# Kernel optimization log

Hardware: AMD Instinct MI355X
Metric: run time of the kernel (lower is better)

## Reference

```python
import jax, jax.numpy as jnp
import numpy as np

DIM, HID = 32, 128
B, H, W = 2, 64, 64

def conv2d(x, w, b=None, pad=0, groups=1):
    out = jax.lax.conv_general_dilated(x, w, (1, 1), [(pad, pad), (pad, pad)],
        dimension_numbers=('NCHW', 'OIHW', 'NCHW'), feature_group_count=groups)
    if b is not None:
        out = out + b[None, :, None, None]
    return out

def gelu(x):
    return jax.nn.gelu(x, approximate=False)  # torch nn.GELU default (erf)

def s_conv(x, dw_w, dw_b, pw_w, pw_b):
    # separable conv: depthwise 3x3 (pad 1) then pointwise 1x1
    y = conv2d(x, dw_w, dw_b, pad=1, groups=x.shape[1])
    return conv2d(y, pw_w, pw_b, pad=0)

def deform_conv2d(x, off_w, off_b, w, b, k, pad):
    # torchvision-style deformable conv, stride 1, zero-padded bilinear sampling
    Bb, C, Hh, Ww = x.shape
    T = k * k
    off = conv2d(x, off_w, off_b, pad=pad).reshape(Bb, T, 2, Hh, Ww)
    dy, dx = off[:, :, 0], off[:, :, 1]                    # [B,T,H,W]
    ky, kx = jnp.meshgrid(jnp.arange(k), jnp.arange(k), indexing='ij')
    py = (jnp.arange(Hh, dtype=x.dtype).reshape(1, 1, Hh, 1)
          + ky.reshape(1, T, 1, 1).astype(x.dtype) - pad + dy)
    px = (jnp.arange(Ww, dtype=x.dtype).reshape(1, 1, 1, Ww)
          + kx.reshape(1, T, 1, 1).astype(x.dtype) - pad + dx)
    y0 = jnp.floor(py); x0 = jnp.floor(px)
    wy = py - y0; wx = px - x0
    y0 = y0.astype(jnp.int32); x0 = x0.astype(jnp.int32)
    flat = x.reshape(Bb, C, Hh * Ww)

    def corner(yi, xi, wgt):
        valid = (yi >= 0) & (yi < Hh) & (xi >= 0) & (xi < Ww)
        idx = jnp.clip(yi, 0, Hh - 1) * Ww + jnp.clip(xi, 0, Ww - 1)
        idx = jnp.broadcast_to(idx.reshape(Bb, 1, T * Hh * Ww), (Bb, C, T * Hh * Ww))
        v = jnp.take_along_axis(flat, idx, axis=2).reshape(Bb, C, T, Hh, Ww)
        return v * jnp.where(valid, wgt, jnp.zeros_like(wgt))[:, None]

    val = (corner(y0, x0, (1 - wy) * (1 - wx)) + corner(y0, x0 + 1, (1 - wy) * wx)
           + corner(y0 + 1, x0, wy * (1 - wx)) + corner(y0 + 1, x0 + 1, wy * wx))
    out = jnp.einsum('bcthw,oct->bohw', val, w.reshape(w.shape[0], C, T))
    return out + b[None, :, None, None]


def setup_inputs() -> dict:
    key = jax.random.key(0)
    ks = iter(jax.random.split(key, 40))
    def rn(shape, scale):
        return jax.random.normal(next(ks), shape, jnp.float32) * scale
    p = {}
    p['x'] = rn((B, H * W, DIM), 1.0)
    p['w1'] = rn((DIM, HID), DIM ** -0.5); p['b1'] = rn((HID,), 0.02)
    p['sc1_dw_w'] = rn((HID, 1, 3, 3), 1.0 / 3.0); p['sc1_dw_b'] = rn((HID,), 0.02)
    p['sc1_pw_w'] = rn((2 * HID, HID, 1, 1), HID ** -0.5); p['sc1_pw_b'] = rn((2 * HID,), 0.02)
    for name, k in (('d3', 7), ('d4', 3), ('d5', 5)):
        p[name + '_off_w'] = rn((2 * k * k, HID, k, k), 0.01 * (HID * k * k) ** -0.5)
        p[name + '_off_b'] = jnp.zeros((2 * k * k,), jnp.float32)
        p[name + '_w'] = rn((HID, HID, k, k), (HID * k * k) ** -0.5)
        p[name + '_b'] = rn((HID,), 0.02)
    p['w2'] = rn((HID, DIM), HID ** -0.5); p['b2'] = rn((DIM,), 0.02)
    return p


def reference(x, w1, b1, sc1_dw_w, sc1_dw_b, sc1_pw_w, sc1_pw_b,
              d3_off_w, d3_off_b, d3_w, d3_b,
              d4_off_w, d4_off_b, d4_w, d4_b,
              d5_off_w, d5_off_b, d5_w, d5_b, w2, b2):
    Bb, HW, C = x.shape
    hh = int(round(HW ** 0.5))
    x1 = gelu(x @ w1 + b1)                                   # [B,HW,HID]
    xi = x1.transpose(0, 2, 1).reshape(Bb, HID, hh, hh)       # b (h w) c -> b c h w
    y = gelu(s_conv(xi, sc1_dw_w, sc1_dw_b, sc1_pw_w, sc1_pw_b))  # [B,2*HID,h,w]
    a, g = jnp.split(y, 2, axis=1)
    a = gelu(deform_conv2d(a, d3_off_w, d3_off_b, d3_w, d3_b, 7, 3))
    a = gelu(deform_conv2d(a, d4_off_w, d4_off_b, d4_w, d4_b, 3, 1))
    a = gelu(deform_conv2d(a, d5_off_w, d5_off_b, d5_w, d5_b, 5, 2))
    z = gelu(a) * g                                           # gated GELU fusion
    z = z.reshape(Bb, HID, HW).transpose(0, 2, 1)             # b c h w -> b (h w) c
    return z @ w2 + b2
```

## Files before the change

kernel.cpp:

```cpp
#include <hip/hip_runtime.h>
#include <hip/hip_bf16.h>

#define HWSZ 4096

typedef _Float16 half8 __attribute__((ext_vector_type(8)));
typedef _Float16 half4 __attribute__((ext_vector_type(4)));
typedef float f32x4 __attribute__((ext_vector_type(4)));

__device__ __forceinline__ float gelu_f(float v) {
    return 0.5f * v * (1.0f + erff(v * 0.7071067811865475f));
}

__device__ __forceinline__ void wtr_elem(const float* __restrict__ w,
                                         _Float16* __restrict__ o,
                                         int i, int T, int Op, int O, float scale) {
    int c = i & 127;
    int op = (i >> 7) % Op;
    int t = i / (128 * Op);
    float v = (op < O) ? w[((size_t)(op * 128 + c)) * T + t] * scale : 0.f;
    o[i] = (_Float16)v;
}

__device__ __forceinline__ void wfrag_elemO(const float* __restrict__ w,
                                            _Float16* __restrict__ o,
                                            int i, int T, int MTt, int O, float scale) {
    int j = i & 7;
    int l = (i >> 3) & 63;
    int cc = (i >> 9) & 3;
    int m = (i >> 11) % MTt;
    int t = i / (2048 * MTt);
    int oc = m * 16 + (l & 15);
    int ch = (l >> 4) * 8 + cc * 32 + j;
    float v = (oc < O) ? w[((size_t)(oc * 128 + ch)) * T + t] * scale : 0.f;
    o[i] = (_Float16)v;
}

__global__ __launch_bounds__(256) void kprep(const float* __restrict__ dww,
                                             const float* __restrict__ pww,
                                             const float* __restrict__ o3w,
                                             const float* __restrict__ d3w,
                                             const float* __restrict__ o4w,
                                             const float* __restrict__ d4w,
                                             const float* __restrict__ o5w,
                                             const float* __restrict__ d5w,
                                             const float* __restrict__ w1,
                                             _Float16* __restrict__ dwt,
                                             _Float16* __restrict__ pwt,
                                             _Float16* __restrict__ wA3,
                                             _Float16* __restrict__ wA4,
                                             _Float16* __restrict__ wA5,
                                             _Float16* __restrict__ wM3,
                                             _Float16* __restrict__ wM4,
                                             _Float16* __restrict__ wM5,
                                             _Float16* __restrict__ wA1,
                                             unsigned int* __restrict__ zbase) {
    int i = blockIdx.x * 256 + threadIdx.x;
    if (i < 1152) {
        int c = i & 127, j = i >> 7;
        dwt[j * 128 + c] = (_Float16)dww[c * 9 + j];
        return;
    }
    i -= 1152;
    if (i < 32768) { pwt[i] = (_Float16)pww[i]; return; }
    i -= 32768;
    if (i < 802816) { wfrag_elemO(o3w, wA3, i, 49, 8, 98, 256.f); return; }
    i -= 802816;
    if (i < 36864) { wfrag_elemO(o4w, wA4, i, 9, 2, 18, 256.f); return; }
    i -= 36864;
    if (i < 204800) { wfrag_elemO(o5w, wA5, i, 25, 4, 50, 256.f); return; }
    i -= 204800;
    if (i < 802816) { wfrag_elemO(d3w, wM3, i, 49, 8, 128, 16.f); return; }
    i -= 802816;
    if (i < 147456) { wfrag_elemO(d4w, wM4, i, 9, 8, 128, 16.f); return; }
    i -= 147456;
    if (i < 409600) { wfrag_elemO(d5w, wM5, i, 25, 8, 128, 16.f); return; }
    i -= 409600;
    if (i < 4096) {
        int k = i & 31, oc = i >> 5;
        wA1[i] = (_Float16)w1[k * 128 + oc];
        return;
    }
    i -= 4096;
    if (i < 1290240) { zbase[i] = 0u; return; }
}

__global__ __launch_bounds__(512) void k1G(const float* __restrict__ x,
                                           const _Float16* __restrict__ wA1,
                                           const float* __restrict__ b1,
                                           _Float16* __restrict__ xicl) {
    int tid = threadIdx.x;
    int wv = tid >> 6;
    int l = tid & 63;
    int col = l & 15, kg = l >> 4;
    int blk = blockIdx.x;
    int b = blk >> 8;
    int p = ((blk & 255) << 4) + col;
    const float* xr = x + ((size_t)(b * HWSZ) + p) * 32 + kg * 8;
    half8 bf;
#pragma unroll
    for (int j = 0; j < 8; ++j) bf[j] = (_Float16)xr[j];
    half8 af = *(const half8*)(wA1 + (wv * 16 + col) * 32 + kg * 8);
    f32x4 acc = (f32x4){0.f, 0.f, 0.f, 0.f};
    acc = __builtin_amdgcn_mfma_f32_16x16x32_f16(af, bf, acc, 0, 0, 0);
    half4 t4;
#pragma unroll
    for (int r = 0; r < 4; ++r) {
        int oc = wv * 16 + kg * 4 + r;
        t4[r] = (_Float16)gelu_f(acc[r] + b1[oc]);
    }
    *(half4*)(xicl + ((size_t)(b * HWSZ) + p) * 128 + wv * 16 + kg * 4) = t4;
}

__global__ __launch_bounds__(256) void k2_cl(const _Float16* __restrict__ xicl,
                                             const _Float16* __restrict__ dwt,
                                             const float* __restrict__ dwb,
                                             _Float16* __restrict__ dcl) {
    int idx = blockIdx.x * 256 + threadIdx.x;
    int cg = idx & 15;
    int p = (idx >> 4) & 4095;
    int b = idx >> 16;
    int h = p >> 6, w = p & 63;
    const _Float16* base = xicl + (size_t)b * HWSZ * 128;
    float acc[8];
#pragma unroll
    for (int j = 0; j < 8; ++j) acc[j] = 0.f;
#pragma unroll
    for (int i = 0; i < 3; ++i) {
        int y = h + i - 1;
        if ((unsigned)y > 63u) continue;
#pragma unroll
        for (int j2 = 0; j2 < 3; ++j2) {
            int xx = w + j2 - 1;
            if ((unsigned)xx > 63u) continue;
            half8 v = *(const half8*)(base + ((size_t)(y * 64 + xx)) * 128 + cg * 8);
            half8 wv8 = *(const half8*)(dwt + (i * 3 + j2) * 128 + cg * 8);
#pragma unroll
            for (int j = 0; j < 8; ++j) acc[j] = fmaf((float)v[j], (float)wv8[j], acc[j]);
        }
    }
    half8 o;
#pragma unroll
    for (int j = 0; j < 8; ++j) o[j] = (_Float16)(acc[j] + dwb[cg * 8 + j]);
    *(half8*)(dcl + ((size_t)(b * HWSZ) + p) * 128 + cg * 8) = o;
}

__global__ __launch_bounds__(512) void k3G(const _Float16* __restrict__ dcl,
                                           const _Float16* __restrict__ pwt,
                                           const float* __restrict__ pwb,
                                           _Float16* __restrict__ clA,
                                           _Float16* __restrict__ gcl) {
    int tid = threadIdx.x;
    int wv = tid >> 6;
    int l = tid & 63;
    int col = l & 15, kg = l >> 4;
    int blk = blockIdx.x;
    int hf = blockIdx.y;
    int b = blk >> 8;
    int px0 = (blk & 255) << 4;
    int p = px0 + col;
    const _Float16* bp = dcl + ((size_t)(b * HWSZ) + p) * 128 + kg * 8;
    int oc0 = hf * 128 + wv * 16;
    const _Float16* ap = pwt + (size_t)(oc0 + col) * 128 + kg * 8;
    f32x4 acc = (f32x4){0.f, 0.f, 0.f, 0.f};
#pragma unroll
    for (int cc = 0; cc < 4; ++cc) {
        half8 bf = *(const half8*)(bp + cc * 32);
        half8 af = *(const half8*)(ap + cc * 32);
        acc = __builtin_amdgcn_mfma_f32_16x16x32_f16(af, bf, acc, 0, 0, 0);
    }
    int h = p >> 6, w = p & 63;
    half4 t4;
#pragma unroll
    for (int r = 0; r < 4; ++r) {
        int oc = oc0 + kg * 4 + r;
        t4[r] = (_Float16)gelu_f(acc[r] + pwb[oc]);
    }
    if (hf == 0) {
        _Float16* dst = clA + (size_t)b * 70 * 72 * 128 +
                        ((size_t)(h + 3) * 72 + (w + 3)) * 128 + wv * 16 + kg * 4;
        *(half4*)dst = t4;
    } else {
        *(half4*)(gcl + ((size_t)(b * HWSZ) + p) * 128 + wv * 16 + kg * 4) = t4;
    }
}

template <int KK, int PAD, int T, int MT, int NG, int NA, int WPX>
__global__ __launch_bounds__(512) void k4Gv4(const _Float16* __restrict__ cl,
                                             const _Float16* __restrict__ wA,
                                             const float* __restrict__ obias,
                                             float* __restrict__ offb, int OC) {
    constexpr int OCp = MT * 16;
    constexpr int COLS = WPX + KK - 1;
    constexpr int NB = 64 / WPX;
    __shared__ _Float16 bS[KK * COLS * 128];

    int tid = threadIdx.x;
    int blk = blockIdx.x;
    int w0 = (blk % NB) * WPX;
    int h = (blk / NB) & 63;
    int b = blk / (NB * 64);
    const _Float16* clb = cl + (size_t)b * 70 * 72 * 128;

    int hh0 = h + (3 - PAD);
    int ww0 = w0 + (3 - PAD);
    for (int g = tid; g < KK * COLS * 16; g += 512) {
        int r = g / (COLS * 16);
        int rest = g - r * (COLS * 16);
        int c = rest >> 4;
        int s = rest & 15;
        half8 v = *(const half8*)(clb + ((size_t)(hh0 + r) * 72 + (ww0 + c)) * 128 + s * 8);
        *(half8*)&bS[((r * COLS + c) * 16 + (s ^ (c & 7))) * 8] = v;
    }

    int wv = tid >> 6;
    int l = tid & 63;
    int col = l & 15, kg = l >> 4;
    int m = wv % MT;
    int ng = wv / MT;

    const half8* apb = (const half8*)wA + (size_t)m * 4 * 64 + l;
    half8 afv[4];
#pragma unroll
    for (int cc = 0; cc < 4; ++cc) afv[cc] = apb[cc * 64];

    f32x4 acc[NA];
#pragma unroll
    for (int a = 0; a < NA; ++a) acc[a] = (f32x4){0.f, 0.f, 0.f, 0.f};

    __syncthreads();

    for (int t = 0; t < T; ++t) {
        int ky = t / KK, kx = t - ky * KK;
        half8 afn[4];
        if (t + 1 < T) {
            const half8* apn = apb + (size_t)(t + 1) * MT * 4 * 64;
#pragma unroll
            for (int cc = 0; cc < 4; ++cc) afn[cc] = apn[cc * 64];
        }
#pragma unroll
        for (int a = 0; a < NA; ++a) {
            int cw = ng * NA * 16 + a * 16 + col + kx;
#pragma unroll
            for (int cc = 0; cc < 4; ++cc) {
                half8 bf = *(const half8*)&bS[((ky * COLS + cw) * 16 + ((cc * 4 + kg) ^ (cw & 7))) * 8];
                acc[a] = __builtin_amdgcn_mfma_f32_16x16x32_f16(afv[cc], bf, acc[a], 0, 0, 0);
            }
        }
#pragma unroll
        for (int cc = 0; cc < 4; ++cc) afv[cc] = afn[cc];
    }

#pragma unroll
    for (int a = 0; a < NA; ++a) {
        int px = h * 64 + w0 + ng * NA * 16 + a * 16 + col;
#pragma unroll
        for (int r = 0; r < 4; ++r) {
            int oc = m * 16 + kg * 4 + r;
            float v = acc[a][r] * (1.0f / 256.0f) + (oc < OC ? obias[oc] : 0.f);
            offb[((size_t)(b * OCp + oc)) * HWSZ + px] = v;
        }
    }
}

template <int KK, int PAD, int T, int NCH>
__global__ __launch_bounds__(512, 4) void k5Gv12(const _Float16* __restrict__ cl,
                                                 const float* __restrict__ offb, int OFFP,
                                                 const _Float16* __restrict__ wM,
                                                 float* __restrict__ pb0,
                                                 float* __restrict__ pb1,
                                                 float* __restrict__ pb2,
                                                 float* __restrict__ pb3) {
    constexpr int ROWS = KK + 2;
    constexpr int COLSW = KK + 17;
    constexpr int UMAX = ((T + NCH - 1) / NCH) * 16;
    __shared__ _Float16 win[ROWS * COLSW * 128];
    __shared__ _Float16 panel[2][16][128];
    __shared__ float pw4[4][UMAX];
    __shared__ int po4[4][UMAX];

    int tid = threadIdx.x;
    int blk = blockIdx.x;
    int chunk = blockIdx.y;
    int base = T / NCH, rem = T % NCH;
    int TS = chunk * base + min(chunk, rem);
    int TE = TS + base + (chunk < rem ? 1 : 0);
    int U = TE - TS;
    int b = blk >> 8;
    int px0 = (blk & 255) << 4;
    int h0 = px0 >> 6;
    int w0 = px0 & 63;
    const _Float16* clb = cl + (size_t)b * 70 * 72 * 128;
    const float* ob = offb + (size_t)b * OFFP * HWSZ;

    int R0 = min(max(h0 - PAD + 2, 0), 68 - KK);
    int C0 = min(max(w0 - PAD + 2, 0), 55 - KK);

    for (int g = tid; g < ROWS * COLSW * 16; g += 512) {
        int r = g / (COLSW * 16);
        int rest = g - r * (COLSW * 16);
        int c = rest >> 4, s = rest & 15;
        *(half8*)&win[((r * COLSW + c) << 7) + s * 8] =
            *(const half8*)(clb + ((size_t)(R0 + r) * 72 + (C0 + c)) * 128 + s * 8);
    }

    for (int q = tid; q < U * 16; q += 512) {
        int t = TS + (q >> 4);
        int px = q & 15;
        int p_s = px0 + px;
        int w_s = w0 + px;
        int ky = t / KK, kx = t - ky * KK;
        float dy = ob[(size_t)(2 * t) * HWSZ + p_s];
        float dx = ob[(size_t)(2 * t + 1) * HWSZ + p_s];
        float py = (float)(h0 + ky - PAD) + dy;
        float pxs = (float)(w_s + kx - PAD) + dx;
        float y0f = floorf(py), x0f = floorf(pxs);
        float wy = py - y0f, wx = pxs - x0f;
        int y0 = (int)y0f, x0 = (int)x0f;
        int y1 = y0 + 1, x1 = x0 + 1;
        bool vy0 = (y0 >= 0) && (y0 < 64), vy1 = (y1 >= 0) && (y1 < 64);
        bool vx0 = (x0 >= 0) && (x0 < 64), vx1 = (x1 >= 0) && (x1 < 64);
        int cy0 = min(max(y0, 0), 63) + 3, cy1 = min(max(y1, 0), 63) + 3;
        int cx0 = min(max(x0, 0), 63) + 3, cx1 = min(max(x1, 0), 63) + 3;
        pw4[0][q] = (vy0 && vx0) ? (1.f - wy) * (1.f - wx) : 0.f;
        pw4[1][q] = (vy0 && vx1) ? (1.f - wy) * wx : 0.f;
        pw4[2][q] = (vy1 && vx0) ? wy * (1.f - wx) : 0.f;
        pw4[3][q] = (vy1 && vx1) ? wy * wx : 0.f;
        po4[0][q] = ((cy0 - R0) * COLSW) << 7;
        po4[1][q] = ((cy1 - R0) * COLSW) << 7;
        po4[2][q] = (cx0 - C0) << 7;
        po4[3][q] = (cx1 - C0) << 7;
    }

    int px_s = tid >> 5;
    int slice4 = tid & 31;
    int wv = tid >> 6;
    int l = tid & 63;
    int col = l & 15, kg = l >> 4;

    f32x4 acc = (f32x4){0.f, 0.f, 0.f, 0.f};
    half8 wA8[4], wB8[4];

    auto BLEND = [&](int t, int buf) {
        int q = (t - TS) * 16 + px_s;
        float w00 = pw4[0][q], w01 = pw4[1][q], w10 = pw4[2][q], w11 = pw4[3][q];
        int o0 = po4[0][q], o1 = po4[1][q], o2 = po4[2][q], o3 = po4[3][q];
        int c0 = slice4 * 4;
        half4 a00 = *(const half4*)(win + o0 + o2 + c0);
        half4 a01 = *(const half4*)(win + o0 + o3 + c0);
        half4 a10 = *(const half4*)(win + o1 + o2 + c0);
        half4 a11 = *(const half4*)(win + o1 + o3 + c0);
        half4 r;
#pragma unroll
        for (int j = 0; j < 4; ++j) {
            float v = w00 * (float)a00[j] + w01 * (float)a01[j] +
                      w10 * (float)a10[j] + w11 * (float)a11[j];
            r[j] = (_Float16)v;
        }
        *(half4*)&panel[buf][px_s][((slice4 >> 1) ^ (px_s & 7)) * 8 + (slice4 & 1) * 4] = r;
    };
    auto LOADW = [&](half8* w8, int t) {
        const half8* ap = (const half8*)wM + ((size_t)(t * 8 + wv) * 4) * 64 + l;
#pragma unroll
        for (int cc = 0; cc < 4; ++cc) w8[cc] = ap[cc * 64];
    };
    auto MM = [&](const half8* w8, int buf) {
#pragma unroll
        for (int cc = 0; cc < 4; ++cc) {
            half8 bf = *(const half8*)&panel[buf][col][((cc * 4 + kg) ^ (col & 7)) * 8];
            acc = __builtin_amdgcn_mfma_f32_16x16x32_f16(w8[cc], bf, acc, 0, 0, 0);
        }
    };
    auto BAR = [&]() {
        asm volatile("s_waitcnt lgkmcnt(0)" ::: "memory");
        __builtin_amdgcn_s_barrier();
        __builtin_amdgcn_sched_barrier(0);
    };

    LOADW(wA8, TS);
    if (TS + 1 < TE) LOADW(wB8, TS + 1);
    BAR();
    BLEND(TS, TS & 1);
    BAR();

    for (int t = TS; t < TE; t += 2) {
        MM(wA8, t & 1);
        if (t + 2 < TE) LOADW(wA8, t + 2);
        if (t + 1 < TE) BLEND(t + 1, (t + 1) & 1);
        BAR();
        if (t + 1 < TE) {
            MM(wB8, (t + 1) & 1);
            if (t + 3 < TE) LOADW(wB8, t + 3);
            if (t + 2 < TE) BLEND(t + 2, (t + 2) & 1);
            BAR();
        }
    }

    float* pb = (chunk == 0) ? pb0 : (chunk == 1) ? pb1 : (chunk == 2) ? pb2 : pb3;
    int p = px0 + col;
    *(f32x4*)&pb[((size_t)(b * HWSZ) + p) * 128 + wv * 16 + kg * 4] = acc;
}

template <int OUTMODE>
__global__ __launch_bounds__(256) void krd4(const float* __restrict__ p0,
                                            const float* __restrict__ p1,
                                            const float* __restrict__ p2,
                                            const float* __restrict__ p3,
                                            const float* __restrict__ bias,
                                            _Float16* __restrict__ outH) {
    int idx = blockIdx.x * 256 + threadIdx.x;
    int oc4 = idx & 31;
    int p = (idx >> 5) & 4095;
    int b = idx >> 17;
    size_t base = ((size_t)(b * HWSZ) + p) * 128 + oc4 * 4;
    f32x4 a = *(const f32x4*)(p0 + base);
    f32x4 c = *(const f32x4*)(p1 + base);
    f32x4 d = *(const f32x4*)(p2 + base);
    f32x4 e = *(const f32x4*)(p3 + base);
    half4 t4;
#pragma unroll
    for (int r = 0; r < 4; ++r) {
        float v = ((a[r] + c[r]) + (d[r] + e[r])) * (1.0f / 16.0f) + bias[oc4 * 4 + r];
        t4[r] = (_Float16)gelu_f(v);
    }
    if (OUTMODE == 0) {
        int h = p >> 6, w = p & 63;
        _Float16* dst = outH + (size_t)b * 70 * 72 * 128 +
                        ((size_t)(h + 3) * 72 + (3 + w)) * 128 + oc4 * 4;
        *(half4*)dst = t4;
    } else {
        *(half4*)(outH + base) = t4;
    }
}

__global__ __launch_bounds__(256) void k6z(const _Float16* __restrict__ a5cl,
                                           const _Float16* __restrict__ gcl,
                                           const float* __restrict__ w2,
                                           const float* __restrict__ b2,
                                           float* __restrict__ out) {
    __shared__ float zs[16][128];
    int tid = threadIdx.x;
    int blk = blockIdx.x;
    int b = blk >> 8;
    int px0 = (blk & 255) << 4;
    int px = tid >> 4, sl = tid & 15;
    size_t rb = ((size_t)(b * HWSZ) + px0 + px) * 128 + sl * 8;
    half8 a = *(const half8*)(a5cl + rb);
    half8 g = *(const half8*)(gcl + rb);
#pragma unroll
    for (int j = 0; j < 8; ++j)
        zs[px][sl * 8 + j] = gelu_f((float)a[j]) * (float)g[j];
    __syncthreads();
    int d2 = (tid & 15) * 2;
    float acc0 = b2[d2], acc1 = b2[d2 + 1];
#pragma unroll 16
    for (int c = 0; c < 128; ++c) {
        float zv = zs[px][c];
        acc0 = fmaf(zv, w2[c * 32 + d2], acc0);
        acc1 = fmaf(zv, w2[c * 32 + d2 + 1], acc1);
    }
    float* o = out + ((size_t)(b * HWSZ) + px0 + px) * 32 + d2;
    o[0] = acc0;
    o[1] = acc1;
}

extern "C" void kernel_launch(void* const* d_in, const int* in_sizes, int n_in,
                              void* d_out, int out_size, void* d_ws, size_t ws_size,
                              hipStream_t stream) {
    const float* x   = (const float*)d_in[0];
    const float* w1  = (const float*)d_in[1];
    const float* b1  = (const float*)d_in[2];
    const float* dww = (const float*)d_in[3];
    const float* dwb = (const float*)d_in[4];
    const float* pww = (const float*)d_in[5];
    const float* pwb = (const float*)d_in[6];
    const float* o3w = (const float*)d_in[7];
    const float* o3b = (const float*)d_in[8];
    const float* d3w = (const float*)d_in[9];
    const float* d3b = (const float*)d_in[10];
    const float* o4w = (const float*)d_in[11];
    const float* o4b = (const float*)d_in[12];
    const float* d4w = (const float*)d_in[13];
    const float* d4b = (const float*)d_in[14];
    const float* o5w = (const float*)d_in[15];
    const float* o5b = (const float*)d_in[16];
    const float* d5w = (const float*)d_in[17];
    const float* d5b = (const float*)d_in[18];
    const float* w2  = (const float*)d_in[19];
    const float* b2  = (const float*)d_in[20];

    float* ws = (float*)d_ws;
    float* offb = ws;
    _Float16* clA  = (_Float16*)(ws + 1048576);
    _Float16* clB  = (_Float16*)(ws + 1693696);
    _Float16* xicl = (_Float16*)(ws + 2338816);
    _Float16* dcl  = (_Float16*)(ws + 2863104);
    _Float16* gcl  = (_Float16*)(ws + 3387392);
    _Float16* a5cl = (_Float16*)(ws + 3911680);
    _Float16* wA3  = (_Float16*)(ws + 4960256);
    _Float16* wA4  = (_Float16*)(ws + 5361664);
    _Float16* wA5  = (_Float16*)(ws + 5380096);
    _Float16* wM3  = (_Float16*)(ws + 5482496);
    _Float16* wM4  = (_Float16*)(ws + 5883904);
    _Float16* wM5  = (_Float16*)(ws + 5957632);
    _Float16* dwt  = (_Float16*)(ws + 6162432);
    _Float16* pwt  = (_Float16*)(ws + 6163008);
    float* pb0 = ws + 6179392;
    float* pb1 = ws + 7227968;
    float* pb2 = ws + 2338816;
    float* pb3 = ws + 8276544;
    _Float16* wA1  = (_Float16*)(ws + 9325120);

    kprep<<<14581, 256, 0, stream>>>(dww, pww, o3w, d3w, o4w, d4w, o5w, d5w, w1,
                                     dwt, pwt, wA3, wA4, wA5, wM3, wM4, wM5, wA1,
                                     (unsigned int*)clA);

    k1G<<<512, 512, 0, stream>>>(x, wA1, b1, xicl);
    k2_cl<<<512, 256, 0, stream>>>(xicl, dwt, dwb, dcl);
    k3G<<<dim3(512, 2), 512, 0, stream>>>(dcl, pwt, pwb, clA, gcl);

    k4Gv4<7, 3, 49, 8, 1, 2, 32><<<256, 512, 0, stream>>>(clA, wA3, o3b, offb, 98);
    k5Gv12<7, 3, 49, 4><<<dim3(512, 4), 512, 0, stream>>>(clA, offb, 128, wM3, pb0, pb1, pb2, pb3);
    krd4<0><<<1024, 256, 0, stream>>>(pb0, pb1, pb2, pb3, d3b, clB);

    k4Gv4<3, 1, 9, 2, 4, 1, 64><<<128, 512, 0, stream>>>(clB, wA4, o4b, offb, 18);
    k5Gv12<3, 1, 9, 4><<<dim3(512, 4), 512, 0, stream>>>(clB, offb, 32, wM4, pb0, pb1, pb2, pb3);
    krd4<0><<<1024, 256, 0, stream>>>(pb0, pb1, pb2, pb3, d4b, clA);

    k4Gv4<5, 2, 25, 4, 2, 1, 32><<<256, 512, 0, stream>>>(clA, wA5, o5b, offb, 50);
    k5Gv12<5, 2, 25, 4><<<dim3(512, 4), 512, 0, stream>>>(clA, offb, 64, wM5, pb0, pb1, pb2, pb3);
    krd4<2><<<1024, 256, 0, stream>>>(pb0, pb1, pb2, pb3, d5b, a5cl);

    k6z<<<512, 256, 0, stream>>>(a5cl, gcl, w2, b2, (float*)d_out);
}
```

Baseline: 191.9 us.

## Fuse deform-conv tap reduction with bias+GELU epilogue, drop split-T partials

Drops the 4-way split of the kernel taps across blockIdx.y, so each block accumulates all taps itself and applies bias and GELU directly. This removes the fp32 partial-sum buffers and the separate reduction kernel after each deformable conv. The sampling offsets are packed into a uchar4 per entry to keep the full-T shared tables small. The trade-off is a quarter as many blocks (512 instead of 2048), each running a longer serial tap loop, so there is less parallelism and latency hiding.

Result: faster. 163.0 us (-15.1%).

```diff
diff --git a/kernel.cpp b/kernel.cpp
--- a/kernel.cpp
+++ b/kernel.cpp
@@ -262,29 +262,22 @@
     }
 }
 
-template <int KK, int PAD, int T, int NCH>
-__global__ __launch_bounds__(512, 4) void k5Gv12(const _Float16* __restrict__ cl,
+template <int KK, int PAD, int T, int OUTMODE>
+__global__ __launch_bounds__(512, 4) void k5Gv13(const _Float16* __restrict__ cl,
                                                  const float* __restrict__ offb, int OFFP,
                                                  const _Float16* __restrict__ wM,
-                                                 float* __restrict__ pb0,
-                                                 float* __restrict__ pb1,
-                                                 float* __restrict__ pb2,
-                                                 float* __restrict__ pb3) {
+                                                 const float* __restrict__ bias,
+                                                 _Float16* __restrict__ outH) {
     constexpr int ROWS = KK + 2;
     constexpr int COLSW = KK + 17;
-    constexpr int UMAX = ((T + NCH - 1) / NCH) * 16;
+    constexpr int UMAX = T * 16;
     __shared__ _Float16 win[ROWS * COLSW * 128];
     __shared__ _Float16 panel[2][16][128];
     __shared__ float pw4[4][UMAX];
-    __shared__ int po4[4][UMAX];
+    __shared__ uchar4 po4[UMAX];
 
     int tid = threadIdx.x;
     int blk = blockIdx.x;
-    int chunk = blockIdx.y;
-    int base = T / NCH, rem = T % NCH;
-    int TS = chunk * base + min(chunk, rem);
-    int TE = TS + base + (chunk < rem ? 1 : 0);
-    int U = TE - TS;
     int b = blk >> 8;
     int px0 = (blk & 255) << 4;
     int h0 = px0 >> 6;
@@ -303,8 +296,8 @@
             *(const half8*)(clb + ((size_t)(R0 + r) * 72 + (C0 + c)) * 128 + s * 8);
     }
 
-    for (int q = tid; q < U * 16; q += 512) {
-        int t = TS + (q >> 4);
+    for (int q = tid; q < T * 16; q += 512) {
+        int t = q >> 4;
         int px = q & 15;
         int p_s = px0 + px;
         int w_s = w0 + px;
@@ -325,10 +318,8 @@
         pw4[1][q] = (vy0 && vx1) ? (1.f - wy) * wx : 0.f;
         pw4[2][q] = (vy1 && vx0) ? wy * (1.f - wx) : 0.f;
         pw4[3][q] = (vy1 && vx1) ? wy * wx : 0.f;
-        po4[0][q] = ((cy0 - R0) * COLSW) << 7;
-        po4[1][q] = ((cy1 - R0) * COLSW) << 7;
-        po4[2][q] = (cx0 - C0) << 7;
-        po4[3][q] = (cx1 - C0) << 7;
+        po4[q] = make_uchar4((unsigned char)(cy0 - R0), (unsigned char)(cy1 - R0),
+                             (unsigned char)(cx0 - C0), (unsigned char)(cx1 - C0));
     }
 
     int px_s = tid >> 5;
@@ -341,9 +332,13 @@
     half8 wA8[4], wB8[4];
 
     auto BLEND = [&](int t, int buf) {
-        int q = (t - TS) * 16 + px_s;
+        int q = t * 16 + px_s;
         float w00 = pw4[0][q], w01 = pw4[1][q], w10 = pw4[2][q], w11 = pw4[3][q];
-        int o0 = po4[0][q], o1 = po4[1][q], o2 = po4[2][q], o3 = po4[3][q];
+        uchar4 pk = po4[q];
+        int o0 = ((int)pk.x * COLSW) << 7;
+        int o1 = ((int)pk.y * COLSW) << 7;
+        int o2 = ((int)pk.z) << 7;
+        int o3 = ((int)pk.w) << 7;
         int c0 = slice4 * 4;
         half4 a00 = *(const half4*)(win + o0 + o2 + c0);
         half4 a01 = *(const half4*)(win + o0 + o3 + c0);
@@ -376,59 +371,39 @@
         __builtin_amdgcn_sched_barrier(0);
     };
 
-    LOADW(wA8, TS);
-    if (TS + 1 < TE) LOADW(wB8, TS + 1);
+    LOADW(wA8, 0);
+    if (1 < T) LOADW(wB8, 1);
     BAR();
-    BLEND(TS, TS & 1);
+    BLEND(0, 0);
     BAR();
 
-    for (int t = TS; t < TE; t += 2) {
+    for (int t = 0; t < T; t += 2) {
         MM(wA8, t & 1);
-        if (t + 2 < TE) LOADW(wA8, t + 2);
-        if (t + 1 < TE) BLEND(t + 1, (t + 1) & 1);
+        if (t + 2 < T) LOADW(wA8, t + 2);
+        if (t + 1 < T) BLEND(t + 1, (t + 1) & 1);
         BAR();
-        if (t + 1 < TE) {
+        if (t + 1 < T) {
             MM(wB8, (t + 1) & 1);
-            if (t + 3 < TE) LOADW(wB8, t + 3);
-            if (t + 2 < TE) BLEND(t + 2, (t + 2) & 1);
+            if (t + 3 < T) LOADW(wB8, t + 3);
+            if (t + 2 < T) BLEND(t + 2, (t + 2) & 1);
             BAR();
         }
     }
 
-    float* pb = (chunk == 0) ? pb0 : (chunk == 1) ? pb1 : (chunk == 2) ? pb2 : pb3;
     int p = px0 + col;
-    *(f32x4*)&pb[((size_t)(b * HWSZ) + p) * 128 + wv * 16 + kg * 4] = acc;
-}
-
-template <int OUTMODE>
-__global__ __launch_bounds__(256) void krd4(const float* __restrict__ p0,
-                                            const float* __restrict__ p1,
-                                            const float* __restrict__ p2,
-                                            const float* __restrict__ p3,
-                                            const float* __restrict__ bias,
-                                            _Float16* __restrict__ outH) {
-    int idx = blockIdx.x * 256 + threadIdx.x;
-    int oc4 = idx & 31;
-    int p = (idx >> 5) & 4095;
-    int b = idx >> 17;
-    size_t base = ((size_t)(b * HWSZ) + p) * 128 + oc4 * 4;
-    f32x4 a = *(const f32x4*)(p0 + base);
-    f32x4 c = *(const f32x4*)(p1 + base);
-    f32x4 d = *(const f32x4*)(p2 + base);
-    f32x4 e = *(const f32x4*)(p3 + base);
     half4 t4;
 #pragma unroll
     for (int r = 0; r < 4; ++r) {
-        float v = ((a[r] + c[r]) + (d[r] + e[r])) * (1.0f / 16.0f) + bias[oc4 * 4 + r];
-        t4[r] = (_Float16)gelu_f(v);
+        int oc = wv * 16 + kg * 4 + r;
+        t4[r] = (_Float16)gelu_f(acc[r] * (1.0f / 16.0f) + bias[oc]);
     }
     if (OUTMODE == 0) {
         int h = p >> 6, w = p & 63;
         _Float16* dst = outH + (size_t)b * 70 * 72 * 128 +
-                        ((size_t)(h + 3) * 72 + (3 + w)) * 128 + oc4 * 4;
+                        ((size_t)(h + 3) * 72 + (3 + w)) * 128 + wv * 16 + kg * 4;
         *(half4*)dst = t4;
     } else {
-        *(half4*)(outH + base) = t4;
+        *(half4*)(outH + ((size_t)(b * HWSZ) + p) * 128 + wv * 16 + kg * 4) = t4;
     }
 }
 
@@ -504,10 +479,6 @@
     _Float16* wM5  = (_Float16*)(ws + 5957632);
     _Float16* dwt  = (_Float16*)(ws + 6162432);
     _Float16* pwt  = (_Float16*)(ws + 6163008);
-    float* pb0 = ws + 6179392;
-    float* pb1 = ws + 7227968;
-    float* pb2 = ws + 2338816;
-    float* pb3 = ws + 8276544;
     _Float16* wA1  = (_Float16*)(ws + 9325120);
 
     kprep<<<14581, 256, 0, stream>>>(dww, pww, o3w, d3w, o4w, d4w, o5w, d5w, w1,
@@ -519,16 +490,13 @@
     k3G<<<dim3(512, 2), 512, 0, stream>>>(dcl, pwt, pwb, clA, gcl);
 
     k4Gv4<7, 3, 49, 8, 1, 2, 32><<<256, 512, 0, stream>>>(clA, wA3, o3b, offb, 98);
-    k5Gv12<7, 3, 49, 4><<<dim3(512, 4), 512, 0, stream>>>(clA, offb, 128, wM3, pb0, pb1, pb2, pb3);
-    krd4<0><<<1024, 256, 0, stream>>>(pb0, pb1, pb2, pb3, d3b, clB);
+    k5Gv13<7, 3, 49, 0><<<512, 512, 0, stream>>>(clA, offb, 128, wM3, d3b, clB);
 
     k4Gv4<3, 1, 9, 2, 4, 1, 64><<<128, 512, 0, stream>>>(clB, wA4, o4b, offb, 18);
-    k5Gv12<3, 1, 9, 4><<<dim3(512, 4), 512, 0, stream>>>(clB, offb, 32, wM4, pb0, pb1, pb2, pb3);
-    krd4<0><<<1024, 256, 0, stream>>>(pb0, pb1, pb2, pb3, d4b, clA);
+    k5Gv13<3, 1, 9, 0><<<512, 512, 0, stream>>>(clB, offb, 32, wM4, d4b, clA);
 
     k4Gv4<5, 2, 25, 4, 2, 1, 32><<<256, 512, 0, stream>>>(clA, wA5, o5b, offb, 50);
-    k5Gv12<5, 2, 25, 4><<<dim3(512, 4), 512, 0, stream>>>(clA, offb, 64, wM5, pb0, pb1, pb2, pb3);
-    krd4<2><<<1024, 256, 0, stream>>>(pb0, pb1, pb2, pb3, d5b, a5cl);
+    k5Gv13<5, 2, 25, 2><<<512, 512, 0, stream>>>(clA, offb, 64, wM5, d5b, a5cl);
 
     k6z<<<512, 256, 0, stream>>>(a5cl, gcl, w2, b2, (float*)d_out);
 }
```
